# Performance work log

Measured on AMD Instinct MI355X. Metric: run time of the kernel, lower is better.

## Reference

```python
import jax, jax.numpy as jnp
import numpy as np

B, L, D = 4, 2048, 1024
NEG = float(-2**32 + 1)  # -4294967295.0, as in the torch source


def setup_inputs() -> dict:
    key = jax.random.key(0)
    k1, k2, k3, k4 = jax.random.split(key, 4)
    # xavier_normal_ std for square DxD weight: sqrt(2/(D+D)) = 1/sqrt(D)
    std = (2.0 / (D + D)) ** 0.5
    return {
        "hidden": jax.random.normal(k1, (B, L, D), dtype=jnp.float32),
        "hyper_embedding": jax.random.normal(k2, (B, L, D), dtype=jnp.float32),
        "W1": jax.random.normal(k3, (D, D), dtype=jnp.float32) * std,
        "b1": jnp.zeros((D,), dtype=jnp.float32),
        "W2": jax.random.normal(k4, (D, D), dtype=jnp.float32) * std,
        "b2": jnp.zeros((D,), dtype=jnp.float32),
    }


def reference(hidden, hyper_embedding, W1, b1, W2, b2):
    _, max_len, dim = hidden.shape
    # nn.Linear: x @ W.T + b
    Q = hyper_embedding @ W1.T + b1          # [B, L, D]
    K = hyper_embedding @ W2.T + b2          # [B, L, D]
    # Q_K[b, m, l] = sum_d Q[b, l, d] * K[b, m, d]
    qk = jnp.einsum('bld,bmd->bml', Q, K)    # [B, L, L]
    qk = qk / (dim ** 0.5 + 1e-6)
    # upper-triangular (including diagonal) additive mask of -2^32+1
    mask = jnp.triu(jnp.full((max_len, max_len), NEG, dtype=qk.dtype), k=0)
    score = jax.nn.softmax(qk + mask[None, :, :], axis=-1)  # [B, L, L]
    # torch.einsum('bll,bmd->bld', score, hidden):
    #   out[b,l,d] = diag(score)[b,l] * sum_m hidden[b,m,d]
    diag = jnp.diagonal(score, axis1=1, axis2=2)            # [B, L]
    hsum = jnp.sum(hidden, axis=1)                          # [B, D]
    return diag[:, :, None] * hsum[:, None, :]              # [B, L, D]
```

## Files before the change

kernel.cpp:

```cpp
#include <hip/hip_runtime.h>


namespace {
constexpr int B = 4;
constexpr int L = 2048;
constexpr int D = 1024;
constexpr int D4 = D / 4;
constexpr int CI = 8;
constexpr int CHUNKS = D4 / CI;
constexpr int WAYS = 256 / CI;
constexpr int NSUM = CHUNKS * B;
constexpr int NZ = 896;
constexpr int NROWS_Z = (L - 1) * B;
}

__global__ __launch_bounds__(256) void k_fused(const float* __restrict__ hidden,
                                               float* __restrict__ out) {
    const int bid = blockIdx.x;
    const int t = threadIdx.x;

    if (bid < NSUM) {
        const int c = bid & (CHUNKS - 1);
        const int b = bid >> 5;
        const int ci = t & (CI - 1);
        const int ri = t >> 3;
        const int colf4 = c * CI + ci;

        const float4* hp = reinterpret_cast<const float4*>(hidden + (size_t)b * L * D);
        float4 s = make_float4(0.f, 0.f, 0.f, 0.f);
#pragma unroll 16
        for (int r = ri; r < L; r += WAYS) {
            float4 v = hp[(size_t)r * D4 + colf4];
            s.x += v.x; s.y += v.y; s.z += v.z; s.w += v.w;
        }

        __shared__ float4 red[256];
        red[t] = s;
        __syncthreads();
#pragma unroll
        for (int sh = WAYS / 2; sh > 0; sh >>= 1) {
            if (ri < sh) {
                float4 o = red[(ri + sh) * CI + ci];
                float4 m = red[t];
                m.x += o.x; m.y += o.y; m.z += o.z; m.w += o.w;
                red[t] = m;
            }
            __syncthreads();
        }
        if (ri == 0) {
            float4 m = red[ci];
            const float sc = 1.0f / (float)L;
            m.x *= sc; m.y *= sc; m.z *= sc; m.w *= sc;
            reinterpret_cast<float4*>(out + (size_t)b * L * D)[colf4] = m;
        }
    } else {
        const int z = bid - NSUM;
        const float4 zero = make_float4(0.f, 0.f, 0.f, 0.f);
        for (int flat = z; flat < NROWS_Z; flat += NZ) {
            const int b = flat / (L - 1);
            const int row = 1 + flat % (L - 1);
            reinterpret_cast<float4*>(out + ((size_t)b * L + row) * D)[t] = zero;
        }
    }
}

extern "C" void kernel_launch(void* const* d_in, const int* in_sizes, int n_in,
                              void* d_out, int out_size, void* d_ws, size_t ws_size,
                              hipStream_t stream) {
    const float* hidden = (const float*)d_in[0];
    float* out = (float*)d_out;
    hipLaunchKernelGGL(k_fused, dim3(NSUM + NZ), dim3(256), 0, stream, hidden, out);
}
```

Baseline: 17.35 us.

## Interleave sum and zero-fill blocks with 512-thread blocks and fewer zero blocks

Raises the block size to 512 threads and interleaves column-sum blocks (even ids) with zero-fill blocks (odd ids), so both memory streams are spread evenly across CUs. The zero-fill path drops from 896 blocks to 128, with each block writing two rows per iteration. Row 0 is skipped by a masking branch instead of per-row div/mod indexing. The grid becomes 256 large blocks, roughly one per CU, which lowers launch count but may leave less parallelism to hide memory latency.

```diff
diff --git a/kernel.cpp b/kernel.cpp
--- a/kernel.cpp
+++ b/kernel.cpp
@@ -6,22 +6,24 @@
 constexpr int L = 2048;
 constexpr int D = 1024;
 constexpr int D4 = D / 4;
+constexpr int NT = 512;
 constexpr int CI = 8;
 constexpr int CHUNKS = D4 / CI;
-constexpr int WAYS = 256 / CI;
+constexpr int WAYS = NT / CI;
 constexpr int NSUM = CHUNKS * B;
-constexpr int NZ = 896;
-constexpr int NROWS_Z = (L - 1) * B;
+constexpr int NZB = 128;
+constexpr int NPAIR = B * L / 2;
 }
 
-__global__ __launch_bounds__(256) void k_fused(const float* __restrict__ hidden,
-                                               float* __restrict__ out) {
+__global__ __launch_bounds__(NT) void k_fused(const float* __restrict__ hidden,
+                                              float* __restrict__ out) {
     const int bid = blockIdx.x;
     const int t = threadIdx.x;
 
-    if (bid < NSUM) {
-        const int c = bid & (CHUNKS - 1);
-        const int b = bid >> 5;
+    if ((bid & 1) == 0) {
+        const int sidx = bid >> 1;
+        const int c = sidx & (CHUNKS - 1);
+        const int b = sidx >> 5;
         const int ci = t & (CI - 1);
         const int ri = t >> 3;
         const int colf4 = c * CI + ci;
@@ -34,7 +36,7 @@
             s.x += v.x; s.y += v.y; s.z += v.z; s.w += v.w;
         }
 
-        __shared__ float4 red[256];
+        __shared__ float4 red[NT];
         red[t] = s;
         __syncthreads();
 #pragma unroll
@@ -54,12 +56,15 @@
             reinterpret_cast<float4*>(out + (size_t)b * L * D)[colf4] = m;
         }
     } else {
-        const int z = bid - NSUM;
+        const int zidx = bid >> 1;
+        const int rp = t >> 8;
+        const int col = t & (D4 - 1);
         const float4 zero = make_float4(0.f, 0.f, 0.f, 0.f);
-        for (int flat = z; flat < NROWS_Z; flat += NZ) {
-            const int b = flat / (L - 1);
-            const int row = 1 + flat % (L - 1);
-            reinterpret_cast<float4*>(out + ((size_t)b * L + row) * D)[t] = zero;
+        for (int p = zidx; p < NPAIR; p += NZB) {
+            const int fr = 2 * p + rp;
+            const int row = fr & (L - 1);
+            if (row > 0)
+                reinterpret_cast<float4*>(out)[(size_t)fr * D4 + col] = zero;
         }
     }
 }
@@ -69,5 +74,5 @@
                               hipStream_t stream) {
     const float* hidden = (const float*)d_in[0];
     float* out = (float*)d_out;
-    hipLaunchKernelGGL(k_fused, dim3(NSUM + NZ), dim3(256), 0, stream, hidden, out);
+    hipLaunchKernelGGL(k_fused, dim3(NSUM + NZB), dim3(NT), 0, stream, hidden, out);
 }
```

After: 14.65 us (median of 2 runs). -15.6%, faster.
